# Optimization experiments

Measured on AMD Instinct MI355X. Metric: run time of the kernel, lower is better.

Reference implementation:

```python
import jax, jax.numpy as jnp
import numpy as np

N_HEAD = 32
N_KV_HEAD = 8
HEAD_DIM = 64
N_EMBD = 2048
B, T = 2, 2048
ROPE_BASE = 10000.0


def _rope_cos_sin(T, head_dim, dtype):
    pos = jnp.arange(T, dtype=jnp.float32)
    dim_arr = jnp.arange(0, head_dim, 2, dtype=jnp.float32)
    freqs = ROPE_BASE ** (-dim_arr / head_dim)
    theta = jnp.outer(pos, freqs)                      # [T, hd/2]
    cos = jnp.concatenate([jnp.cos(theta), jnp.cos(theta)], axis=-1)  # [T, hd]
    sin = jnp.concatenate([jnp.sin(theta), jnp.sin(theta)], axis=-1)
    # broadcast to [1, T, 1, hd]
    return cos[None, :, None, :].astype(dtype), sin[None, :, None, :].astype(dtype)


def _rotate_half(v):
    h = v.shape[-1] // 2
    return jnp.concatenate([-v[..., h:], v[..., :h]], axis=-1)


def setup_inputs() -> dict:
    key = jax.random.key(0)
    kx, kq, kk, kv, ko = jax.random.split(key, 5)
    s = 1.0 / np.sqrt(N_EMBD)
    return {
        "x": jax.random.normal(kx, (B, T, N_EMBD), dtype=jnp.float32),
        "wq": jax.random.normal(kq, (N_EMBD, N_HEAD * HEAD_DIM), dtype=jnp.float32) * s,
        "wk": jax.random.normal(kk, (N_EMBD, N_KV_HEAD * HEAD_DIM), dtype=jnp.float32) * s,
        "wv": jax.random.normal(kv, (N_EMBD, N_KV_HEAD * HEAD_DIM), dtype=jnp.float32) * s,
        "wo": jax.random.normal(ko, (N_HEAD * HEAD_DIM, N_EMBD), dtype=jnp.float32) * s,
    }


def reference(x, wq, wk, wv, wo):
    Bx, Tx, C = x.shape
    n_rep = N_HEAD // N_KV_HEAD

    xq = (x @ wq).reshape(Bx, Tx, N_HEAD, HEAD_DIM)
    xk = (x @ wk).reshape(Bx, Tx, N_KV_HEAD, HEAD_DIM)
    xv = (x @ wv).reshape(Bx, Tx, N_KV_HEAD, HEAD_DIM)

    cos, sin = _rope_cos_sin(Tx, HEAD_DIM, x.dtype)
    xq = xq * cos + _rotate_half(xq) * sin
    xk = xk * cos + _rotate_half(xk) * sin

    # GQA: repeat_interleave KV heads to match query heads
    xk = jnp.repeat(xk, n_rep, axis=2)  # [B, T, H, hd]
    xv = jnp.repeat(xv, n_rep, axis=2)

    scale = 1.0 / np.sqrt(HEAD_DIM)
    # scores: [B, H, T, T]
    scores = jnp.einsum("bqhd,bkhd->bhqk", xq, xk) * scale
    causal = jnp.tril(jnp.ones((Tx, Tx), dtype=bool))
    scores = jnp.where(causal[None, None], scores, -jnp.inf)
    probs = jax.nn.softmax(scores, axis=-1)

    out = jnp.einsum("bhqk,bkhd->bqhd", probs, xv).reshape(Bx, Tx, N_HEAD * HEAD_DIM)
    return out @ wo
```

## Files before the change

kernel.cpp:

```cpp
#include <hip/hip_runtime.h>
#include <hip/hip_bf16.h>
#include <cstdint>
#include <cstddef>

#define B_ 2
#define T_ 2048
#define H_ 32
#define KVH_ 8
#define D_ 64
#define C_ 2048
#define NQKV 3072

typedef short short8 __attribute__((ext_vector_type(8)));
typedef float f32x4 __attribute__((ext_vector_type(4)));
typedef unsigned short u16;

__device__ __forceinline__ u16 f2b(float f) {
  union { float f; unsigned u; } x; x.f = f;
  unsigned r = x.u + 0x7fffu + ((x.u >> 16) & 1u);
  return (u16)(r >> 16);
}

__device__ __forceinline__ float b2f(u16 v) {
  union { unsigned u; float f; } x; x.u = ((unsigned)v) << 16;
  return x.f;
}

__device__ __forceinline__ void gload16(const void* g, void* l) {
  __builtin_amdgcn_global_load_lds(
      (const __attribute__((address_space(1))) unsigned int*)g,
      (__attribute__((address_space(3))) unsigned int*)l,
      16, 0, 0);
}

__device__ __forceinline__ f32x4 mfma16(short8 a, short8 b, f32x4 c) {
  return __builtin_amdgcn_mfma_f32_16x16x32_bf16(a, b, c, 0, 0, 0);
}

__device__ __forceinline__ unsigned cvtpk(float lo_, float hi_) {
  unsigned r;
  asm("v_cvt_pk_bf16_f32 %0, %1, %2" : "=v"(r) : "v"(lo_), "v"(hi_));
  return r;
}

__global__ void k_tbl(float* __restrict__ tbl) {
  int i = blockIdx.x * 256 + threadIdx.x;
  int t = i >> 5, f = i & 31;
  double freq = pow(10000.0, -(double)f / 32.0);
  double th = (double)t * freq;
  tbl[i * 2 + 0] = (float)cos(th);
  tbl[i * 2 + 1] = (float)sin(th);
}

__global__ void k_cvtx(const float* __restrict__ x, u16* __restrict__ xb) {
  int i = blockIdx.x * 256 + threadIdx.x;
  float4 v = ((const float4*)x)[i];
  ushort4 o;
  o.x = f2b(v.x); o.y = f2b(v.y); o.z = f2b(v.z); o.w = f2b(v.w);
  ((ushort4*)xb)[i] = o;
}

__global__ void k_transw(const float* __restrict__ src, u16* __restrict__ dst, int N) {
  __shared__ float t[32][33];
  int tx = threadIdx.x, ty = threadIdx.y;
  int k0 = blockIdx.y * 32, n0 = blockIdx.x * 32;
#pragma unroll
  for (int i = 0; i < 4; i++)
    t[ty + i * 8][tx] = src[(size_t)(k0 + ty + i * 8) * N + n0 + tx];
  __syncthreads();
#pragma unroll
  for (int i = 0; i < 4; i++) {
    int nl = ty + i * 8;
    dst[(size_t)(n0 + nl) * 2048 + k0 + tx] = f2b(t[tx][nl]);
  }
}

template <bool BF16OUT>
__global__ __launch_bounds__(256, 2) void k_gemm(const u16* __restrict__ A,
                                                 const u16* __restrict__ Bt,
                                                 void* __restrict__ Cc,
                                                 int M, int N, int K) {
  __shared__ __align__(16) u16 As[128 * 64];
  __shared__ __align__(16) u16 Bs[128 * 64];
  const int tid = threadIdx.x;
  const int w = tid >> 6, l = tid & 63;
  const int lo = l & 15, hi = l >> 4;
  const int m0 = blockIdx.y * 128, n0 = blockIdx.x * 128;
  const int wr = w >> 1, wc = w & 1;
  f32x4 acc[4][4];
#pragma unroll
  for (int i = 0; i < 4; i++)
#pragma unroll
    for (int j = 0; j < 4; j++) acc[i][j] = (f32x4){0.f, 0.f, 0.f, 0.f};

  for (int k0 = 0; k0 < K; k0 += 64) {
#pragma unroll
    for (int i = 0; i < 4; i++) {
      int cid = i * 256 + tid;
      int row = cid >> 3, kc = cid & 7;
      gload16(A + (size_t)(m0 + row) * K + k0 + kc * 8, &As[(i * 256 + w * 64) * 8]);
      gload16(Bt + (size_t)(n0 + row) * K + k0 + kc * 8, &Bs[(i * 256 + w * 64) * 8]);
    }
    __syncthreads();
#pragma unroll
    for (int kk = 0; kk < 2; kk++) {
      short8 a[4], b[4];
#pragma unroll
      for (int i = 0; i < 4; i++)
        a[i] = *(const short8*)&As[(wr * 64 + i * 16 + lo) * 64 + kk * 32 + hi * 8];
#pragma unroll
      for (int j = 0; j < 4; j++)
        b[j] = *(const short8*)&Bs[(wc * 64 + j * 16 + lo) * 64 + kk * 32 + hi * 8];
#pragma unroll
      for (int i = 0; i < 4; i++)
#pragma unroll
        for (int j = 0; j < 4; j++) acc[i][j] = mfma16(a[i], b[j], acc[i][j]);
    }
    __syncthreads();
  }
  const int r0 = m0 + wr * 64, c0 = n0 + wc * 64;
#pragma unroll
  for (int i = 0; i < 4; i++)
#pragma unroll
    for (int j = 0; j < 4; j++) {
      f32x4 v = acc[i][j];
      int col = c0 + j * 16 + lo;
      int rw = r0 + i * 16 + hi * 4;
#pragma unroll
      for (int r = 0; r < 4; r++) {
        if (BF16OUT)
          ((u16*)Cc)[(size_t)(rw + r) * N + col] = f2b(v[r]);
        else
          ((float*)Cc)[(size_t)(rw + r) * N + col] = v[r];
      }
    }
}

__global__ void k_rope(const u16* __restrict__ QKV, const float* __restrict__ tbl,
                       u16* __restrict__ Qb, u16* __restrict__ Kb, u16* __restrict__ Vb) {
  int bt = blockIdx.x;
  int b = bt >> 11, t = bt & 2047;
  const u16* row = QKV + (size_t)bt * NQKV;
  const float2* cs = (const float2*)tbl + (size_t)t * 32;
  int tid = threadIdx.x;
  const float QS = 0.125f * 1.44269504089f;
#pragma unroll
  for (int i = 0; i < 4; i++) {
    int p = i * 256 + tid;
    int h = p >> 5, dd = p & 31;
    float2 c = cs[dd];
    float q0 = b2f(row[h * 64 + dd]), q1 = b2f(row[h * 64 + dd + 32]);
    float o0 = (q0 * c.x - q1 * c.y) * QS;
    float o1 = (q1 * c.x + q0 * c.y) * QS;
    size_t base = ((size_t)(b * H_ + h) * T_ + t) * 64 + dd;
    Qb[base] = f2b(o0);
    Qb[base + 32] = f2b(o1);
  }
  {
    int kvh = tid >> 5, dd = tid & 31;
    float2 c = cs[dd];
    float k0v = b2f(row[2048 + kvh * 64 + dd]), k1v = b2f(row[2048 + kvh * 64 + dd + 32]);
    size_t base = ((size_t)(b * KVH_ + kvh) * T_ + t) * 64 + dd;
    Kb[base] = f2b(k0v * c.x - k1v * c.y);
    Kb[base + 32] = f2b(k1v * c.x + k0v * c.y);
  }
#pragma unroll
  for (int i = 0; i < 2; i++) {
    int e = i * 256 + tid;
    int kvh = e >> 6, dd = e & 63;
    Vb[((size_t)(b * KVH_ + kvh) * T_ + t) * 64 + dd] = row[2560 + e];
  }
}

__global__ void k_vtrans(const u16* __restrict__ Vb, u16* __restrict__ Vt) {
  __shared__ u16 tl[64][65];
  int bk = blockIdx.y;
  int t0 = blockIdx.x * 64;
  int tid = threadIdx.x;
#pragma unroll
  for (int i = 0; i < 16; i++) {
    int e = i * 256 + tid;
    int tlc = e >> 6, d = e & 63;
    tl[tlc][d] = Vb[((size_t)bk * T_ + t0 + tlc) * 64 + d];
  }
  __syncthreads();
#pragma unroll
  for (int i = 0; i < 16; i++) {
    int e = i * 256 + tid;
    int d = e >> 6, tc = e & 63;
    Vt[((size_t)bk * 64 + d) * T_ + t0 + tc] = tl[tc][d];
  }
}

#define PSTR 40
__global__ __launch_bounds__(256)
__attribute__((amdgpu_waves_per_eu(3, 3)))
void k_attn(const u16* __restrict__ Qb,
            const u16* __restrict__ Kb,
            const u16* __restrict__ Vt,
            u16* __restrict__ Ob) {
  __shared__ __align__(16) u16 Pl[4][2][16 * PSTR];
  const int tid = threadIdx.x, w = tid >> 6, l = tid & 63;
  const int lo = l & 15, hi = l >> 4;
  const int b = blockIdx.z, h = blockIdx.y, kvh = h >> 2;
  const int p = (int)blockIdx.x * 4 + w;

  const size_t qbase = (size_t)(b * H_ + h) * T_ * 64;
  const size_t kbase = (size_t)(b * KVH_ + kvh) * T_ * 64;
  const size_t vbase = (size_t)(b * KVH_ + kvh) * 64 * T_;

  for (int pass = 0; pass < 2; pass++) {
    const int tile = pass ? (63 - p) : p;
    const int q0 = tile * 32;

    const u16* kptr = Kb + kbase + (size_t)lo * 64 + hi * 8;
    const u16* vp[4];
#pragma unroll
    for (int jd = 0; jd < 4; jd++)
      vp[jd] = Vt + vbase + (size_t)(jd * 16 + lo) * T_ + hi * 8;

    short8 aq[2][2];
#pragma unroll
    for (int qt = 0; qt < 2; qt++)
#pragma unroll
      for (int hf = 0; hf < 2; hf++)
        aq[qt][hf] = *(const short8*)&Qb[qbase + (size_t)(q0 + qt * 16 + lo) * 64 + hf * 32 + hi * 8];

    f32x4 o[2][4];
    float m[2], lsum[2];
#pragma unroll
    for (int qt = 0; qt < 2; qt++) {
      m[qt] = -1e30f; lsum[qt] = 0.f;
#pragma unroll
      for (int jd = 0; jd < 4; jd++) o[qt][jd] = (f32x4){0.f, 0.f, 0.f, 0.f};
    }

    auto LOADK = [&](short8 (&ak)[2][2]) {
      ak[0][0] = *(const short8*)(kptr);
      ak[0][1] = *(const short8*)(kptr + 32);
      ak[1][0] = *(const short8*)(kptr + 1024);
      ak[1][1] = *(const short8*)(kptr + 1056);
      kptr += 2048;
    };

    auto STEP = [&](const short8 (&ak)[2][2], int kv0, bool masked) {
      short8 av[4];
#pragma unroll
      for (int jd = 0; jd < 4; jd++) {
        av[jd] = *(const short8*)vp[jd];
        vp[jd] += 32;
      }

      f32x4 s[2][2];
      __builtin_amdgcn_s_setprio(1);
#pragma unroll
      for (int qt = 0; qt < 2; qt++)
#pragma unroll
        for (int f = 0; f < 2; f++) {
          f32x4 acc = (f32x4){0.f, 0.f, 0.f, 0.f};
          acc = mfma16(ak[f][0], aq[qt][0], acc);
          acc = mfma16(ak[f][1], aq[qt][1], acc);
          s[qt][f] = acc;
        }
      __builtin_amdgcn_s_setprio(0);

#pragma unroll
      for (int qt = 0; qt < 2; qt++) {
        const int myq = q0 + qt * 16 + lo;
        float p_[8];
#pragma unroll
        for (int f = 0; f < 2; f++)
#pragma unroll
          for (int r = 0; r < 4; r++) {
            float v = s[qt][f][r];
            if (masked) {
              int kv = kv0 + f * 16 + hi * 4 + r;
              v = (kv <= myq) ? v : -1e30f;
            }
            p_[f * 4 + r] = v;
          }
        float mx = fmaxf(fmaxf(fmaxf(p_[0], p_[1]), fmaxf(p_[2], p_[3])),
                         fmaxf(fmaxf(p_[4], p_[5]), fmaxf(p_[6], p_[7])));
        mx = fmaxf(mx, __shfl_xor(mx, 16));
        mx = fmaxf(mx, __shfl_xor(mx, 32));
        if (!__all(mx <= m[qt] + 11.5f)) {
          float mn = fmaxf(m[qt], mx);
          float a_ = exp2f(m[qt] - mn);
          m[qt] = mn;
          lsum[qt] *= a_;
#pragma unroll
          for (int jd = 0; jd < 4; jd++) {
            f32x4 t = o[qt][jd];
#pragma unroll
            for (int r = 0; r < 4; r++) t[r] *= a_;
            o[qt][jd] = t;
          }
        }
        float sm = 0.f;
#pragma unroll
        for (int i = 0; i < 8; i++) { p_[i] = exp2f(p_[i] - m[qt]); sm += p_[i]; }
        sm += __shfl_xor(sm, 16);
        sm += __shfl_xor(sm, 32);
        lsum[qt] += sm;
        uint2 w0, w1;
        w0.x = cvtpk(p_[0], p_[1]); w0.y = cvtpk(p_[2], p_[3]);
        w1.x = cvtpk(p_[4], p_[5]); w1.y = cvtpk(p_[6], p_[7]);
        *(uint2*)&Pl[w][qt][lo * PSTR + hi * 4] = w0;
        *(uint2*)&Pl[w][qt][lo * PSTR + 16 + hi * 4] = w1;
      }

#pragma unroll
      for (int qt = 0; qt < 2; qt++) {
        short8 pb = *(const short8*)&Pl[w][qt][lo * PSTR + hi * 8];
        __builtin_amdgcn_s_setprio(1);
#pragma unroll
        for (int jd = 0; jd < 4; jd++) o[qt][jd] = mfma16(av[jd], pb, o[qt][jd]);
        __builtin_amdgcn_s_setprio(0);
      }
    };

    short8 akA[2][2], akB[2][2];
    LOADK(akA);
    int kv0 = 0;
    while (kv0 + 64 <= q0) {
      LOADK(akB);
      STEP(akA, kv0, false);
      LOADK(akA);
      STEP(akB, kv0 + 32, false);
      kv0 += 64;
    }
    if (kv0 < q0) {
      LOADK(akB);
      STEP(akA, kv0, false);
      STEP(akB, q0, true);
    } else {
      STEP(akA, q0, true);
    }

#pragma unroll
    for (int qt = 0; qt < 2; qt++) {
      const int myq = q0 + qt * 16 + lo;
      float inv = 1.0f / lsum[qt];
      size_t obase = ((size_t)(b * T_ + myq) * H_ + h) * 64;
#pragma unroll
      for (int jd = 0; jd < 4; jd++) {
        ushort4 ov;
        ov.x = f2b(o[qt][jd][0] * inv);
        ov.y = f2b(o[qt][jd][1] * inv);
        ov.z = f2b(o[qt][jd][2] * inv);
        ov.w = f2b(o[qt][jd][3] * inv);
        *(ushort4*)&Ob[obase + jd * 16 + hi * 4] = ov;
      }
    }
  }
}

constexpr size_t OFF_TBL = 0;
constexpr size_t SZ_TBL = (size_t)T_ * 32 * 2 * 4;
constexpr size_t OFF_XB = OFF_TBL + SZ_TBL;
constexpr size_t SZ_XB = (size_t)B_ * T_ * C_ * 2;
constexpr size_t OFF_WQKVT = OFF_XB + SZ_XB;
constexpr size_t SZ_WQKVT = (size_t)NQKV * C_ * 2;
constexpr size_t OFF_WOT = OFF_WQKVT + SZ_WQKVT;
constexpr size_t SZ_WOT = (size_t)C_ * C_ * 2;
constexpr size_t OFF_QKV = OFF_WOT + SZ_WOT;
constexpr size_t SZ_QKV = (size_t)B_ * T_ * NQKV * 2;
constexpr size_t OFF_QB = OFF_QKV + SZ_QKV;
constexpr size_t SZ_QB = (size_t)B_ * H_ * T_ * D_ * 2;
constexpr size_t OFF_KB = OFF_QB + SZ_QB;
constexpr size_t SZ_KVB = (size_t)B_ * KVH_ * T_ * D_ * 2;
constexpr size_t OFF_VB = OFF_KB + SZ_KVB;
constexpr size_t OFF_VT = OFF_VB + SZ_KVB;
constexpr size_t OFF_OB = OFF_VT + SZ_KVB;
constexpr size_t SZ_OB = (size_t)B_ * T_ * H_ * D_ * 2;

extern "C" void kernel_launch(void* const* d_in, const int* in_sizes, int n_in,
                              void* d_out, int out_size, void* d_ws, size_t ws_size,
                              hipStream_t stream) {
  const float* x = (const float*)d_in[0];
  const float* wq = (const float*)d_in[1];
  const float* wk = (const float*)d_in[2];
  const float* wv = (const float*)d_in[3];
  const float* wo = (const float*)d_in[4];

  char* ws = (char*)d_ws;
  float* tbl = (float*)(ws + OFF_TBL);
  u16* xb = (u16*)(ws + OFF_XB);
  u16* wqkvT = (u16*)(ws + OFF_WQKVT);
  u16* woT = (u16*)(ws + OFF_WOT);
  u16* qkv = (u16*)(ws + OFF_QKV);
  u16* Qb = (u16*)(ws + OFF_QB);
  u16* Kb = (u16*)(ws + OFF_KB);
  u16* Vb = (u16*)(ws + OFF_VB);
  u16* Vt = (u16*)(ws + OFF_VT);
  u16* Ob = (u16*)(ws + OFF_OB);

  k_tbl<<<256, 256, 0, stream>>>(tbl);
  k_cvtx<<<8192, 256, 0, stream>>>(x, xb);
  dim3 tb(32, 8);
  k_transw<<<dim3(64, 64), tb, 0, stream>>>(wq, wqkvT, 2048);
  k_transw<<<dim3(16, 64), tb, 0, stream>>>(wk, wqkvT + (size_t)2048 * 2048, 512);
  k_transw<<<dim3(16, 64), tb, 0, stream>>>(wv, wqkvT + (size_t)2560 * 2048, 512);
  k_transw<<<dim3(64, 64), tb, 0, stream>>>(wo, woT, 2048);

  k_gemm<true><<<dim3(NQKV / 128, (B_ * T_) / 128), 256, 0, stream>>>(
      xb, wqkvT, qkv, B_ * T_, NQKV, C_);
  k_rope<<<B_ * T_, 256, 0, stream>>>(qkv, tbl, Qb, Kb, Vb);
  k_vtrans<<<dim3(T_ / 64, B_ * KVH_), 256, 0, stream>>>(Vb, Vt);
  k_attn<<<dim3(8, H_, B_), 256, 0, stream>>>(Qb, Kb, Vt, Ob);
  k_gemm<false><<<dim3(C_ / 128, (B_ * T_) / 128), 256, 0, stream>>>(
      Ob, woT, d_out, B_ * T_, C_, C_);
}
```

Before: 274.3 us.

## Process 64 keys per attention step and drop the K double-buffer prefetch

```diff
diff --git a/kernel.cpp b/kernel.cpp
--- a/kernel.cpp
+++ b/kernel.cpp
@@ -199,7 +199,7 @@
             const u16* __restrict__ Kb,
             const u16* __restrict__ Vt,
             u16* __restrict__ Ob) {
-  __shared__ __align__(16) u16 Pl[4][2][16 * PSTR];
+  __shared__ __align__(16) u16 Pl[4][2][2][16 * PSTR];
   const int tid = threadIdx.x, w = tid >> 6, l = tid & 63;
   const int lo = l & 15, hi = l >> 4;
   const int b = blockIdx.z, h = blockIdx.y, kvh = h >> 2;
@@ -213,12 +213,6 @@
     const int tile = pass ? (63 - p) : p;
     const int q0 = tile * 32;
 
-    const u16* kptr = Kb + kbase + (size_t)lo * 64 + hi * 8;
-    const u16* vp[4];
-#pragma unroll
-    for (int jd = 0; jd < 4; jd++)
-      vp[jd] = Vt + vbase + (size_t)(jd * 16 + lo) * T_ + hi * 8;
-
     short8 aq[2][2];
 #pragma unroll
     for (int qt = 0; qt < 2; qt++)
@@ -235,28 +229,26 @@
       for (int jd = 0; jd < 4; jd++) o[qt][jd] = (f32x4){0.f, 0.f, 0.f, 0.f};
     }
 
-    auto LOADK = [&](short8 (&ak)[2][2]) {
-      ak[0][0] = *(const short8*)(kptr);
-      ak[0][1] = *(const short8*)(kptr + 32);
-      ak[1][0] = *(const short8*)(kptr + 1024);
-      ak[1][1] = *(const short8*)(kptr + 1056);
-      kptr += 2048;
-    };
-
-    auto STEP = [&](const short8 (&ak)[2][2], int kv0, bool masked) {
-      short8 av[4];
-#pragma unroll
-      for (int jd = 0; jd < 4; jd++) {
-        av[jd] = *(const short8*)vp[jd];
-        vp[jd] += 32;
-      }
-
-      f32x4 s[2][2];
+    auto STEP = [&](int kv0, bool masked) {
+      short8 ak[4][2];
+#pragma unroll
+      for (int f = 0; f < 4; f++)
+#pragma unroll
+        for (int hf = 0; hf < 2; hf++)
+          ak[f][hf] = *(const short8*)&Kb[kbase + (size_t)(kv0 + f * 16 + lo) * 64 + hf * 32 + hi * 8];
+      short8 av[2][4];
+#pragma unroll
+      for (int kvh2 = 0; kvh2 < 2; kvh2++)
+#pragma unroll
+        for (int jd = 0; jd < 4; jd++)
+          av[kvh2][jd] = *(const short8*)&Vt[vbase + (size_t)(jd * 16 + lo) * T_ + kv0 + kvh2 * 32 + hi * 8];
+
+      f32x4 s[2][4];
       __builtin_amdgcn_s_setprio(1);
 #pragma unroll
       for (int qt = 0; qt < 2; qt++)
 #pragma unroll
-        for (int f = 0; f < 2; f++) {
+        for (int f = 0; f < 4; f++) {
           f32x4 acc = (f32x4){0.f, 0.f, 0.f, 0.f};
           acc = mfma16(ak[f][0], aq[qt][0], acc);
           acc = mfma16(ak[f][1], aq[qt][1], acc);
@@ -267,9 +259,9 @@
 #pragma unroll
       for (int qt = 0; qt < 2; qt++) {
         const int myq = q0 + qt * 16 + lo;
-        float p_[8];
-#pragma unroll
-        for (int f = 0; f < 2; f++)
+        float p_[16];
+#pragma unroll
+        for (int f = 0; f < 4; f++)
 #pragma unroll
           for (int r = 0; r < 4; r++) {
             float v = s[qt][f][r];
@@ -279,8 +271,11 @@
             }
             p_[f * 4 + r] = v;
           }
-        float mx = fmaxf(fmaxf(fmaxf(p_[0], p_[1]), fmaxf(p_[2], p_[3])),
-                         fmaxf(fmaxf(p_[4], p_[5]), fmaxf(p_[6], p_[7])));
+        float mx = fmaxf(
+            fmaxf(fmaxf(fmaxf(p_[0], p_[1]), fmaxf(p_[2], p_[3])),
+                  fmaxf(fmaxf(p_[4], p_[5]), fmaxf(p_[6], p_[7]))),
+            fmaxf(fmaxf(fmaxf(p_[8], p_[9]), fmaxf(p_[10], p_[11])),
+                  fmaxf(fmaxf(p_[12], p_[13]), fmaxf(p_[14], p_[15]))));
         mx = fmaxf(mx, __shfl_xor(mx, 16));
         mx = fmaxf(mx, __shfl_xor(mx, 32));
         if (!__all(mx <= m[qt] + 11.5f)) {
@@ -298,44 +293,37 @@
         }
         float sm = 0.f;
 #pragma unroll
-        for (int i = 0; i < 8; i++) { p_[i] = exp2f(p_[i] - m[qt]); sm += p_[i]; }
+        for (int i = 0; i < 16; i++) { p_[i] = exp2f(p_[i] - m[qt]); sm += p_[i]; }
         sm += __shfl_xor(sm, 16);
         sm += __shfl_xor(sm, 32);
         lsum[qt] += sm;
-        uint2 w0, w1;
-        w0.x = cvtpk(p_[0], p_[1]); w0.y = cvtpk(p_[2], p_[3]);
-        w1.x = cvtpk(p_[4], p_[5]); w1.y = cvtpk(p_[6], p_[7]);
-        *(uint2*)&Pl[w][qt][lo * PSTR + hi * 4] = w0;
-        *(uint2*)&Pl[w][qt][lo * PSTR + 16 + hi * 4] = w1;
+#pragma unroll
+        for (int half = 0; half < 2; half++) {
+          uint2 w0, w1;
+          w0.x = cvtpk(p_[half * 8 + 0], p_[half * 8 + 1]);
+          w0.y = cvtpk(p_[half * 8 + 2], p_[half * 8 + 3]);
+          w1.x = cvtpk(p_[half * 8 + 4], p_[half * 8 + 5]);
+          w1.y = cvtpk(p_[half * 8 + 6], p_[half * 8 + 7]);
+          *(uint2*)&Pl[w][qt][half][lo * PSTR + hi * 4] = w0;
+          *(uint2*)&Pl[w][qt][half][lo * PSTR + 16 + hi * 4] = w1;
+        }
       }
 
 #pragma unroll
       for (int qt = 0; qt < 2; qt++) {
-        short8 pb = *(const short8*)&Pl[w][qt][lo * PSTR + hi * 8];
-        __builtin_amdgcn_s_setprio(1);
-#pragma unroll
-        for (int jd = 0; jd < 4; jd++) o[qt][jd] = mfma16(av[jd], pb, o[qt][jd]);
-        __builtin_amdgcn_s_setprio(0);
+#pragma unroll
+        for (int kvh2 = 0; kvh2 < 2; kvh2++) {
+          short8 pb = *(const short8*)&Pl[w][qt][kvh2][lo * PSTR + hi * 8];
+          __builtin_amdgcn_s_setprio(1);
+#pragma unroll
+          for (int jd = 0; jd < 4; jd++) o[qt][jd] = mfma16(av[kvh2][jd], pb, o[qt][jd]);
+          __builtin_amdgcn_s_setprio(0);
+        }
       }
     };
 
-    short8 akA[2][2], akB[2][2];
-    LOADK(akA);
-    int kv0 = 0;
-    while (kv0 + 64 <= q0) {
-      LOADK(akB);
-      STEP(akA, kv0, false);
-      LOADK(akA);
-      STEP(akB, kv0 + 32, false);
-      kv0 += 64;
-    }
-    if (kv0 < q0) {
-      LOADK(akB);
-      STEP(akA, kv0, false);
-      STEP(akB, q0, true);
-    } else {
-      STEP(akA, q0, true);
-    }
+    const int nb = tile / 2 + 1;
+    for (int kb = 0; kb < nb; kb++) STEP(kb * 64, kb == nb - 1);
 
 #pragma unroll
     for (int qt = 0; qt < 2; qt++) {
```

After: 275.7 us. About the same (+0.5%).
